# Kernel optimization log

Hardware: AMD Instinct MI355X
Metric: run time of the kernel (lower is better)

Reference implementation:

```python
import jax, jax.numpy as jnp
import numpy as np

N, D_IN, D_OUT, E = 8192, 2048, 8192, 8


def setup_inputs() -> dict:
    key = jax.random.key(0)
    k1, k2, k3 = jax.random.split(key, 3)
    x = jax.random.normal(k1, (N, D_IN), dtype=jnp.float32)
    # packed weight layout [E, in, out] (pack() pretransposes [E,out,in] -> [E,in,out])
    weight = jax.random.normal(k2, (E, D_IN, D_OUT), dtype=jnp.float32) * (1.0 / np.sqrt(D_IN))
    indices = jax.random.randint(k3, (N,), 0, E, dtype=jnp.int32)
    return {"x": x, "weight": weight, "indices": indices}


def reference(x, weight, indices):
    # gather_mm: out[n] = x[n] @ weight[indices[n]]  -> [N, D_OUT]
    # Avoid materializing weight[indices] ([N, in, out]); instead loop over the
    # small fixed expert count, masking tokens routed to each expert.
    n_experts = weight.shape[0]
    out = jnp.zeros((x.shape[0], weight.shape[-1]), dtype=x.dtype)
    for e in range(n_experts):
        mask = (indices == e)[:, None]
        xe = jnp.where(mask, x, 0)          # zero out tokens not routed to e
        out = out + xe @ weight[e]           # [N, in] @ [in, out]
    return out
```

## Files before the change

kernel.cpp:

```cpp
#include <hip/hip_runtime.h>
#include <hip/hip_bf16.h>
#include <stdint.h>

#define N_TOK 8192
#define D_IN  2048
#define D_OUT 8192
#define NEXP  8
#define KST   32
#define NT2   40
#define NS2   32
#define AIMG  32768
#define X_OFF2 65536
#define X_BYTES2 ((long)NT2 * KST * AIMG)
#define W_OFF2 (X_OFF2 + X_BYTES2)
#define W_BYTES2 ((long)NEXP * NS2 * KST * AIMG)
#define WS_NEED2 ((size_t)(W_OFF2 + W_BYTES2))
#define NWIMG (NEXP * 64 * KST)


typedef float  f32x4  __attribute__((ext_vector_type(4)));
typedef __bf16 bf16x8 __attribute__((ext_vector_type(8)));

__global__ void SwitchLinear_setup_kernel(const int* __restrict__ idx,
                                          int* __restrict__ ws) {
    __shared__ int cnt[NEXP], cur[NEXP];
    int t = threadIdx.x;
    if (t < NEXP) cnt[t] = 0;
    __syncthreads();
    for (int i = t; i < N_TOK; i += 256) atomicAdd(&cnt[idx[i]], 1);
    __syncthreads();
    if (t == 0) {
        int o = 0, nt = 0, nt1 = 0;
        for (int e = 0; e < NEXP; ++e) {
            cur[e] = o;
            int c = cnt[e];
            for (int r = 0; r < c; r += 256) {
                ws[8 + nt]   = e;
                ws[96 + nt]  = o + r;
                ws[192 + nt] = (c - r < 256) ? (c - r) : 256;
                ++nt;
            }
            for (int r = 0; r < c; r += 128) {
                ws[256 + nt1] = e;
                ws[328 + nt1] = o + r;
                ws[400 + nt1] = (c - r < 128) ? (c - r) : 128;
                ++nt1;
            }
            o += c;
        }
        ws[0] = nt;
        ws[4] = nt1;
    }
    __syncthreads();
    for (int i = t; i < N_TOK; i += 256) {
        int p = atomicAdd(&cur[idx[i]], 1);
        ws[512 + p] = i;
    }
}

__global__ __launch_bounds__(256) void SwitchLinear_conv_kernel(
    const float* __restrict__ x, const float* __restrict__ w,
    const int* __restrict__ ws, char* __restrict__ wsb) {
    const int bidx = blockIdx.x;
    const int t = threadIdx.x;
    if (bidx < NWIMG) {
        const int img = bidx;
        const int kst = img & 31, s = (img >> 5) & 63, e = img >> 11;
        const int y = s >> 1, hh = s & 1;
        __shared__ float tl[64 * 129];
        const float* src = w + (long)e * D_IN * D_OUT + (long)(kst * 64) * D_OUT +
                           y * 256 + hh * 128;
#pragma unroll
        for (int i = 0; i < 8; ++i) {
            int u = t + i * 256;
            int row = u >> 5, ch = u & 31;
            f32x4 v = *(const f32x4*)(src + (long)row * D_OUT + ch * 4);
            float* d = &tl[row * 129 + ch * 4];
            d[0] = v[0]; d[1] = v[1]; d[2] = v[2]; d[3] = v[3];
        }
        __syncthreads();
        char* dimg = wsb + W_OFF2 + (long)((e * NS2 + y) * KST + kst) * AIMG;
#pragma unroll
        for (int i = 0; i < 4; ++i) {
            int u = t + i * 256;
            int cl = u >> 3, kc8 = u & 7;
            union { __bf16 h8[8]; uint4 u4; } c;
#pragma unroll
            for (int j = 0; j < 8; ++j) c.h8[j] = (__bf16)tl[(kc8 * 8 + j) * 129 + cl];
            int cc = hh * 128 + cl;
            int slot = (((cc & 1) << 2) | (kc8 & 3)) ^ ((cc >> 1) & 7);
            *(uint4*)(dimg + (kc8 >> 2) * 16384 + ((cc >> 1) << 7) + (slot << 4)) = c.u4;
        }
    } else {
        const int u2 = bidx - NWIMG;
        const int tile = u2 % NT2, kst = u2 / NT2;
        if (tile >= ws[0]) return;
        const int rs = ws[96 + tile], rows = ws[192 + tile];
        char* img = wsb + X_OFF2 + (long)(tile * KST + kst) * AIMG;
#pragma unroll
        for (int i = 0; i < 8; ++i) {
            int u = t + i * 256;
            int R = u >> 3, kc8 = u & 7;
            int rl = rs + (R < rows ? R : rows - 1);
            int token = ws[512 + rl];
            const float* src = x + (long)token * D_IN + kst * 64 + kc8 * 8;
            f32x4 v0 = *(const f32x4*)src;
            f32x4 v1 = *(const f32x4*)(src + 4);
            union { __bf16 hh[8]; uint4 u4; } c;
            c.hh[0] = (__bf16)v0[0]; c.hh[1] = (__bf16)v0[1];
            c.hh[2] = (__bf16)v0[2]; c.hh[3] = (__bf16)v0[3];
            c.hh[4] = (__bf16)v1[0]; c.hh[5] = (__bf16)v1[1];
            c.hh[6] = (__bf16)v1[2]; c.hh[7] = (__bf16)v1[3];
            int slot = (((R & 1) << 2) | (kc8 & 3)) ^ ((R >> 1) & 7);
            *(uint4*)(img + (kc8 >> 2) * 16384 + ((R >> 1) << 7) + (slot << 4)) = c.u4;
        }
    }
}


__global__ __launch_bounds__(512, 1) void SwitchLinear_gemm_kernel(
    const char* __restrict__ wsb, const int* __restrict__ ws,
    float* __restrict__ out) {
    const int bid = blockIdx.x;
    const int lb  = (bid & 7) * ((NT2 * NS2) / 8) + (bid >> 3);
    const int tx  = lb % NT2;
    const int y   = lb / NT2;
    if (tx >= ws[0]) return;
    const int e = ws[8 + tx], rs = ws[96 + tx], rows = ws[192 + tx];

    __shared__ __align__(16) char lds[2][2][2][16384];
    __shared__ int ord[256];

    const int t = threadIdx.x;
    if (t < 256) ord[t] = ws[512 + rs + (t < rows ? t : 0)];
    __syncthreads();

    const char* aImg = wsb + X_OFF2 + (long)(tx * KST) * AIMG;
    const char* bImg = wsb + W_OFF2 + (long)((e * NS2 + y) * KST) * AIMG;

    const int lane = t & 63;
    const int wid  = t >> 6;
    const int wr = wid >> 2, wc = wid & 3;
    const int lm = lane & 15, lk = lane >> 4;

    f32x4 acc[8][4];
#pragma unroll
    for (int i = 0; i < 8; ++i)
#pragma unroll
        for (int j = 0; j < 4; ++j) acc[i][j] = (f32x4){0.f, 0.f, 0.f, 0.f};

    bf16x8 aa[4], bb[4];

#define STG(op, ks, half, tt)                                                 \
    __builtin_amdgcn_global_load_lds(                                         \
        (const __attribute__((address_space(1))) uint32_t*)(                  \
            ((op) ? bImg : aImg) + (long)(tt) * AIMG + (ks) * 16384 +         \
            (half) * 8192 + t * 16),                                          \
        (__attribute__((address_space(3))) uint32_t*)(                        \
            &lds[(tt) & 1][op][ks][(half) * 8192 + t * 16]),                  \
        16, 0, 0)

#define SWB(r) ((((r) >> 1) << 7) + (((((((r) & 1) << 2)) | lk) ^ (((r) >> 1) & 7)) << 4))

#define LDB(p, ks)                                                            \
    do { _Pragma("unroll")                                                    \
        for (int ni = 0; ni < 4; ++ni) {                                      \
            int cc = wc * 64 + ni * 16 + lm;                                  \
            bb[ni] = *(const bf16x8*)(&lds[p][1][ks][SWB(cc)]);               \
        } } while (0)

#define LDA(p, ks, mh)                                                        \
    do { _Pragma("unroll")                                                    \
        for (int q = 0; q < 4; ++q) {                                         \
            int rr = wr * 128 + (mh) * 64 + q * 16 + lm;                      \
            aa[q] = *(const bf16x8*)(&lds[p][0][ks][SWB(rr)]);                \
        } } while (0)

#define MFMA16(mh)                                                            \
    do { _Pragma("unroll")                                                    \
        for (int q = 0; q < 4; ++q)                                           \
            _Pragma("unroll")                                                 \
            for (int ni = 0; ni < 4; ++ni)                                    \
                acc[(mh) * 4 + q][ni] = __builtin_amdgcn_mfma_f32_16x16x32_bf16( \
                    aa[q], bb[ni], acc[(mh) * 4 + q][ni], 0, 0, 0);           \
    } while (0)

#define PH(p, ks, mh, DOB, ISSUE, POST)                                       \
    do {                                                                      \
        if (DOB) LDB(p, ks);                                                  \
        LDA(p, ks, mh);                                                       \
        ISSUE;                                                                \
        __builtin_amdgcn_s_barrier();                                         \
        asm volatile("s_waitcnt lgkmcnt(0)" ::: "memory");                    \
        __builtin_amdgcn_sched_barrier(0);                                    \
        __builtin_amdgcn_s_setprio(1);                                        \
        MFMA16(mh);                                                           \
        __builtin_amdgcn_s_setprio(0);                                        \
        POST;                                                                 \
        __builtin_amdgcn_s_barrier();                                         \
    } while (0)

    STG(0, 0, 0, 0); STG(0, 0, 1, 0); STG(1, 0, 0, 0); STG(1, 0, 1, 0);
    STG(0, 1, 0, 0); STG(0, 1, 1, 0); STG(1, 1, 0, 0); STG(1, 1, 1, 0);
    asm volatile("s_waitcnt vmcnt(4)" ::: "memory");
    __builtin_amdgcn_s_barrier();

    for (int tt = 0; tt < KST - 1; ++tt) {
        const int p = tt & 1;
        const int nx = tt + 1;
        PH(p, 0, 0, 1, { STG(0, 0, 0, nx); STG(0, 0, 1, nx); }, ((void)0));
        PH(p, 0, 1, 0, { STG(1, 0, 0, nx); STG(1, 0, 1, nx); },
           asm volatile("s_waitcnt vmcnt(4)" ::: "memory"));
        PH(p, 1, 0, 1, { STG(0, 1, 0, nx); STG(0, 1, 1, nx); }, ((void)0));
        PH(p, 1, 1, 0, { STG(1, 1, 0, nx); STG(1, 1, 1, nx); },
           asm volatile("s_waitcnt vmcnt(4)" ::: "memory"));
    }
    {
        const int p = (KST - 1) & 1;
        PH(p, 0, 0, 1, ((void)0), ((void)0));
        PH(p, 0, 1, 0, ((void)0),
           asm volatile("s_waitcnt vmcnt(0)" ::: "memory"));
        PH(p, 1, 0, 1, ((void)0), ((void)0));
        PH(p, 1, 1, 0, ((void)0), ((void)0));
    }

#pragma unroll
    for (int mi = 0; mi < 8; ++mi) {
#pragma unroll
        for (int j = 0; j < 4; ++j) {
            int rl = wr * 128 + mi * 16 + lk * 4 + j;
            if (rl < rows) {
                int token = ord[rl];
                float* po = out + (long)token * D_OUT + y * 256 + wc * 64 + lm;
#pragma unroll
                for (int ni = 0; ni < 4; ++ni) po[ni * 16] = acc[mi][ni][j];
            }
        }
    }
#undef STG
#undef SWB
#undef LDB
#undef LDA
#undef MFMA16
#undef PH
}


__device__ __forceinline__ int fb_a_byte(int r, int kbyte) {
    return r * 128 + (kbyte ^ ((r & 7) << 4));
}
__device__ __forceinline__ int fb_b_byte(int n, int kbyte) {
    int slot = (n ^ (n >> 2)) & 7;
    return n * 128 + (kbyte ^ (slot << 4));
}

__global__ __launch_bounds__(256, 2) void SwitchLinear_gemm_fb_kernel(
    const float* __restrict__ x, const float* __restrict__ w,
    const int* __restrict__ ws, float* __restrict__ out) {
    const int nt = ws[4];
    const int tx = blockIdx.x;
    if (tx >= nt) return;
    const int e    = ws[256 + tx];
    const int rs   = ws[328 + tx];
    const int rows = ws[400 + tx];
    const int col0 = blockIdx.y * 128;

    __shared__ __align__(16) unsigned short As[128 * 64];
    __shared__ __align__(16) unsigned short Bs[128 * 64];
    __shared__ int ord[128];

    const int t = threadIdx.x;
    if (t < 128) {
        int r = (t < rows) ? (rs + t) : rs;
        ord[t] = ws[512 + r];
    }
    __syncthreads();

    const int kq = t & 15;
    const float* pA[8];
    int rowA[8];
#pragma unroll
    for (int i = 0; i < 8; ++i) {
        int r = (t >> 4) + 16 * i;
        rowA[i] = r;
        pA[i] = x + (long)ord[r] * D_IN + kq * 4;
    }
    const float* pB[2];
    int nB[2], kbB[2];
#pragma unroll
    for (int i = 0; i < 2; ++i) {
        int u = t + 256 * i;
        int kgf = u >> 5, q = u & 31;
        kbB[i] = kgf * 4;
        nB[i]  = q * 4;
        pB[i]  = w + (long)e * D_IN * D_OUT + (long)(kgf * 4) * D_OUT + col0 + q * 4;
    }

    const int lane = t & 63;
    const int wid  = t >> 6;
    const int wr = wid >> 1, wc = wid & 1;
    const int lm = lane & 15, lk = lane >> 4;

    f32x4 acc[4][4];
#pragma unroll
    for (int i = 0; i < 4; ++i)
#pragma unroll
        for (int j = 0; j < 4; ++j) acc[i][j] = (f32x4){0.f, 0.f, 0.f, 0.f};

    for (int k0 = 0; k0 < D_IN; k0 += 64) {
#pragma unroll
        for (int i = 0; i < 8; ++i) {
            f32x4 v = *(const f32x4*)(pA[i] + k0);
            union { __bf16 h[4]; uint2 u; } c;
            c.h[0] = (__bf16)v[0]; c.h[1] = (__bf16)v[1];
            c.h[2] = (__bf16)v[2]; c.h[3] = (__bf16)v[3];
            *(uint2*)((char*)As + fb_a_byte(rowA[i], kq * 8)) = c.u;
        }
#pragma unroll
        for (int i = 0; i < 2; ++i) {
            const float* p = pB[i] + (long)k0 * D_OUT;
            f32x4 r0 = *(const f32x4*)(p);
            f32x4 r1 = *(const f32x4*)(p + D_OUT);
            f32x4 r2 = *(const f32x4*)(p + 2 * D_OUT);
            f32x4 r3 = *(const f32x4*)(p + 3 * D_OUT);
#pragma unroll
            for (int j = 0; j < 4; ++j) {
                int n = nB[i] + j;
                union { __bf16 h[4]; uint2 u; } c;
                c.h[0] = (__bf16)r0[j]; c.h[1] = (__bf16)r1[j];
                c.h[2] = (__bf16)r2[j]; c.h[3] = (__bf16)r3[j];
                *(uint2*)((char*)Bs + fb_b_byte(n, kbB[i] * 2)) = c.u;
            }
        }
        __syncthreads();
#pragma unroll
        for (int ks = 0; ks < 2; ++ks) {
            bf16x8 a[4], b[4];
            const int kbyte = ks * 64 + lk * 16;
#pragma unroll
            for (int mi = 0; mi < 4; ++mi) {
                int r = wr * 64 + mi * 16 + lm;
                a[mi] = *(const bf16x8*)((const char*)As + fb_a_byte(r, kbyte));
            }
#pragma unroll
            for (int ni = 0; ni < 4; ++ni) {
                int n = wc * 64 + ni * 16 + lm;
                b[ni] = *(const bf16x8*)((const char*)Bs + fb_b_byte(n, kbyte));
            }
#pragma unroll
            for (int mi = 0; mi < 4; ++mi)
#pragma unroll
                for (int ni = 0; ni < 4; ++ni)
                    acc[mi][ni] = __builtin_amdgcn_mfma_f32_16x16x32_bf16(
                        a[mi], b[ni], acc[mi][ni], 0, 0, 0);
        }
        __syncthreads();
    }
#pragma unroll
    for (int mi = 0; mi < 4; ++mi) {
#pragma unroll
        for (int j = 0; j < 4; ++j) {
            int rl = wr * 64 + mi * 16 + lk * 4 + j;
            if (rl < rows) {
                int token = ord[rl];
                float* po = out + (long)token * D_OUT + col0 + wc * 64 + lm;
#pragma unroll
                for (int ni = 0; ni < 4; ++ni) po[ni * 16] = acc[mi][ni][j];
            }
        }
    }
}

extern "C" void kernel_launch(void* const* d_in, const int* in_sizes, int n_in,
                              void* d_out, int out_size, void* d_ws, size_t ws_size,
                              hipStream_t stream) {
    const float* x   = (const float*)d_in[0];
    const float* w   = (const float*)d_in[1];
    const int*   idx = (const int*)d_in[2];
    float* out = (float*)d_out;
    int*   ws  = (int*)d_ws;
    char*  wsb = (char*)d_ws;

    SwitchLinear_setup_kernel<<<1, 256, 0, stream>>>(idx, ws);
    if (ws_size >= WS_NEED2) {
        SwitchLinear_conv_kernel<<<NWIMG + NT2 * KST, 256, 0, stream>>>(x, w, ws, wsb);
        SwitchLinear_gemm_kernel<<<NT2 * NS2, 512, 0, stream>>>(wsb, ws, out);
    } else {
        dim3 grid(72, 64);
        SwitchLinear_gemm_fb_kernel<<<grid, 256, 0, stream>>>(x, w, ws, out);
    }
}
```

Baseline: 553.0 us.

## Shrink GEMM tile to 128x128 with 256 threads and two blocks per CU

The main GEMM moves from 256x256 tiles with 512 threads and one block per CU to 128x128 tiles with 256 threads and two blocks per CU. Each tile reads its half of the existing bf16 X and W images, using a new per-tile image index computed in setup. The token order list moves to offset 1024 so the new index table has room. This is meant to reduce padding waste on partial expert tiles and improve load balance and occupancy, at the cost of lower data reuse per tile and more global traffic.

```diff
diff --git a/kernel.cpp b/kernel.cpp
--- a/kernel.cpp
+++ b/kernel.cpp
@@ -8,7 +8,9 @@
 #define NEXP  8
 #define KST   32
 #define NT2   40
+#define NT1G  72
 #define NS2   32
+#define NS1   64
 #define AIMG  32768
 #define X_OFF2 65536
 #define X_BYTES2 ((long)NT2 * KST * AIMG)
@@ -16,6 +18,7 @@
 #define W_BYTES2 ((long)NEXP * NS2 * KST * AIMG)
 #define WS_NEED2 ((size_t)(W_OFF2 + W_BYTES2))
 #define NWIMG (NEXP * 64 * KST)
+#define GRID1 (NT1G * NS1)
 
 
 typedef float  f32x4  __attribute__((ext_vector_type(4)));
@@ -34,17 +37,20 @@
         for (int e = 0; e < NEXP; ++e) {
             cur[e] = o;
             int c = cnt[e];
+            const int T0 = nt;
             for (int r = 0; r < c; r += 256) {
                 ws[8 + nt]   = e;
                 ws[96 + nt]  = o + r;
                 ws[192 + nt] = (c - r < 256) ? (c - r) : 256;
                 ++nt;
             }
+            int j = 0;
             for (int r = 0; r < c; r += 128) {
                 ws[256 + nt1] = e;
                 ws[328 + nt1] = o + r;
                 ws[400 + nt1] = (c - r < 128) ? (c - r) : 128;
-                ++nt1;
+                ws[472 + nt1] = (T0 + (j >> 1)) * 2 + (j & 1);
+                ++nt1; ++j;
             }
             o += c;
         }
@@ -54,7 +60,7 @@
     __syncthreads();
     for (int i = t; i < N_TOK; i += 256) {
         int p = atomicAdd(&cur[idx[i]], 1);
-        ws[512 + p] = i;
+        ws[1024 + p] = i;
     }
 }
 
@@ -102,7 +108,7 @@
             int u = t + i * 256;
             int R = u >> 3, kc8 = u & 7;
             int rl = rs + (R < rows ? R : rows - 1);
-            int token = ws[512 + rl];
+            int token = ws[1024 + rl];
             const float* src = x + (long)token * D_IN + kst * 64 + kc8 * 8;
             f32x4 v0 = *(const f32x4*)src;
             f32x4 v1 = *(const f32x4*)(src + 4);
@@ -118,127 +124,133 @@
 }
 
 
-__global__ __launch_bounds__(512, 1) void SwitchLinear_gemm_kernel(
+__global__ __launch_bounds__(256, 2) void SwitchLinear_gemm_kernel(
     const char* __restrict__ wsb, const int* __restrict__ ws,
     float* __restrict__ out) {
     const int bid = blockIdx.x;
-    const int lb  = (bid & 7) * ((NT2 * NS2) / 8) + (bid >> 3);
-    const int tx  = lb % NT2;
-    const int y   = lb / NT2;
-    if (tx >= ws[0]) return;
-    const int e = ws[8 + tx], rs = ws[96 + tx], rows = ws[192 + tx];
-
-    __shared__ __align__(16) char lds[2][2][2][16384];
-    __shared__ int ord[256];
+    const int lb  = (bid & 7) * (GRID1 / 8) + (bid >> 3);
+    const int tx  = lb % NT1G;
+    const int y   = lb / NT1G;
+    if (tx >= ws[4]) return;
+    const int e = ws[256 + tx], rs = ws[328 + tx], rows = ws[400 + tx];
+    const int img = ws[472 + tx];
+
+    __shared__ __align__(16) char ldsA[2][2][8192];
+    __shared__ __align__(16) char ldsB[2][2][8192];
+    __shared__ int ord[128];
 
     const int t = threadIdx.x;
-    if (t < 256) ord[t] = ws[512 + rs + (t < rows ? t : 0)];
+    if (t < 128) ord[t] = ws[1024 + rs + (t < rows ? t : 0)];
     __syncthreads();
 
-    const char* aImg = wsb + X_OFF2 + (long)(tx * KST) * AIMG;
-    const char* bImg = wsb + W_OFF2 + (long)((e * NS2 + y) * KST) * AIMG;
+    const char* aBase = wsb + X_OFF2 + (long)((img >> 1) * KST) * AIMG + (img & 1) * 8192;
+    const char* bBase = wsb + W_OFF2 + (long)((e * NS2 + (y >> 1)) * KST) * AIMG +
+                        (y & 1) * 8192;
 
     const int lane = t & 63;
     const int wid  = t >> 6;
-    const int wr = wid >> 2, wc = wid & 3;
+    const int wr = wid >> 1, wc = wid & 1;
     const int lm = lane & 15, lk = lane >> 4;
 
-    f32x4 acc[8][4];
-#pragma unroll
-    for (int i = 0; i < 8; ++i)
+    f32x4 acc[4][4];
+#pragma unroll
+    for (int i = 0; i < 4; ++i)
 #pragma unroll
         for (int j = 0; j < 4; ++j) acc[i][j] = (f32x4){0.f, 0.f, 0.f, 0.f};
 
     bf16x8 aa[4], bb[4];
 
-#define STG(op, ks, half, tt)                                                 \
+#define STGA(ks, o2, tt)                                                      \
     __builtin_amdgcn_global_load_lds(                                         \
         (const __attribute__((address_space(1))) uint32_t*)(                  \
-            ((op) ? bImg : aImg) + (long)(tt) * AIMG + (ks) * 16384 +         \
-            (half) * 8192 + t * 16),                                          \
+            aBase + (long)(tt) * AIMG + (ks) * 16384 + (o2) * 4096 + t * 16), \
         (__attribute__((address_space(3))) uint32_t*)(                        \
-            &lds[(tt) & 1][op][ks][(half) * 8192 + t * 16]),                  \
+            &ldsA[(tt) & 1][ks][(o2) * 4096 + t * 16]),                       \
         16, 0, 0)
 
-#define SWB(r) ((((r) >> 1) << 7) + (((((((r) & 1) << 2)) | lk) ^ (((r) >> 1) & 7)) << 4))
+#define STGB(ks, o2, tt)                                                      \
+    __builtin_amdgcn_global_load_lds(                                         \
+        (const __attribute__((address_space(1))) uint32_t*)(                  \
+            bBase + (long)(tt) * AIMG + (ks) * 16384 + (o2) * 4096 + t * 16), \
+        (__attribute__((address_space(3))) uint32_t*)(                        \
+            &ldsB[(tt) & 1][ks][(o2) * 4096 + t * 16]),                       \
+        16, 0, 0)
+
+#define SWBH(r) ((((r) >> 1) << 7) + (((((((r) & 1) << 2)) | lk) ^ (((r) >> 1) & 7)) << 4))
 
 #define LDB(p, ks)                                                            \
     do { _Pragma("unroll")                                                    \
         for (int ni = 0; ni < 4; ++ni) {                                      \
             int cc = wc * 64 + ni * 16 + lm;                                  \
-            bb[ni] = *(const bf16x8*)(&lds[p][1][ks][SWB(cc)]);               \
+            bb[ni] = *(const bf16x8*)(&ldsB[p][ks][SWBH(cc)]);                \
         } } while (0)
 
-#define LDA(p, ks, mh)                                                        \
+#define LDA(p, ks)                                                            \
     do { _Pragma("unroll")                                                    \
         for (int q = 0; q < 4; ++q) {                                         \
-            int rr = wr * 128 + (mh) * 64 + q * 16 + lm;                      \
-            aa[q] = *(const bf16x8*)(&lds[p][0][ks][SWB(rr)]);                \
+            int rr = wr * 64 + q * 16 + lm;                                   \
+            aa[q] = *(const bf16x8*)(&ldsA[p][ks][SWBH(rr)]);                 \
         } } while (0)
 
-#define MFMA16(mh)                                                            \
+#define MFMA16()                                                              \
     do { _Pragma("unroll")                                                    \
         for (int q = 0; q < 4; ++q)                                           \
             _Pragma("unroll")                                                 \
             for (int ni = 0; ni < 4; ++ni)                                    \
-                acc[(mh) * 4 + q][ni] = __builtin_amdgcn_mfma_f32_16x16x32_bf16( \
-                    aa[q], bb[ni], acc[(mh) * 4 + q][ni], 0, 0, 0);           \
+                acc[q][ni] = __builtin_amdgcn_mfma_f32_16x16x32_bf16(         \
+                    aa[q], bb[ni], acc[q][ni], 0, 0, 0);                      \
     } while (0)
 
-#define PH(p, ks, mh, DOB, ISSUE, POST)                                       \
+#define PH(p, ks, ISSUE, POST)                                                \
     do {                                                                      \
-        if (DOB) LDB(p, ks);                                                  \
-        LDA(p, ks, mh);                                                       \
+        LDB(p, ks);                                                           \
+        LDA(p, ks);                                                           \
         ISSUE;                                                                \
         __builtin_amdgcn_s_barrier();                                         \
         asm volatile("s_waitcnt lgkmcnt(0)" ::: "memory");                    \
         __builtin_amdgcn_sched_barrier(0);                                    \
         __builtin_amdgcn_s_setprio(1);                                        \
-        MFMA16(mh);                                                           \
+        MFMA16();                                                             \
         __builtin_amdgcn_s_setprio(0);                                        \
         POST;                                                                 \
         __builtin_amdgcn_s_barrier();                                         \
     } while (0)
 
-    STG(0, 0, 0, 0); STG(0, 0, 1, 0); STG(1, 0, 0, 0); STG(1, 0, 1, 0);
-    STG(0, 1, 0, 0); STG(0, 1, 1, 0); STG(1, 1, 0, 0); STG(1, 1, 1, 0);
+    STGA(0, 0, 0); STGA(0, 1, 0); STGB(0, 0, 0); STGB(0, 1, 0);
+    STGA(1, 0, 0); STGA(1, 1, 0); STGB(1, 0, 0); STGB(1, 1, 0);
     asm volatile("s_waitcnt vmcnt(4)" ::: "memory");
     __builtin_amdgcn_s_barrier();
 
     for (int tt = 0; tt < KST - 1; ++tt) {
         const int p = tt & 1;
         const int nx = tt + 1;
-        PH(p, 0, 0, 1, { STG(0, 0, 0, nx); STG(0, 0, 1, nx); }, ((void)0));
-        PH(p, 0, 1, 0, { STG(1, 0, 0, nx); STG(1, 0, 1, nx); },
+        PH(p, 0, { STGA(0, 0, nx); STGA(0, 1, nx); STGB(0, 0, nx); STGB(0, 1, nx); },
            asm volatile("s_waitcnt vmcnt(4)" ::: "memory"));
-        PH(p, 1, 0, 1, { STG(0, 1, 0, nx); STG(0, 1, 1, nx); }, ((void)0));
-        PH(p, 1, 1, 0, { STG(1, 1, 0, nx); STG(1, 1, 1, nx); },
+        PH(p, 1, { STGA(1, 0, nx); STGA(1, 1, nx); STGB(1, 0, nx); STGB(1, 1, nx); },
            asm volatile("s_waitcnt vmcnt(4)" ::: "memory"));
     }
     {
         const int p = (KST - 1) & 1;
-        PH(p, 0, 0, 1, ((void)0), ((void)0));
-        PH(p, 0, 1, 0, ((void)0),
-           asm volatile("s_waitcnt vmcnt(0)" ::: "memory"));
-        PH(p, 1, 0, 1, ((void)0), ((void)0));
-        PH(p, 1, 1, 0, ((void)0), ((void)0));
-    }
-
-#pragma unroll
-    for (int mi = 0; mi < 8; ++mi) {
+        PH(p, 0, ((void)0), asm volatile("s_waitcnt vmcnt(0)" ::: "memory"));
+        PH(p, 1, ((void)0), ((void)0));
+    }
+
+#pragma unroll
+    for (int mi = 0; mi < 4; ++mi) {
 #pragma unroll
         for (int j = 0; j < 4; ++j) {
-            int rl = wr * 128 + mi * 16 + lk * 4 + j;
+            int rl = wr * 64 + mi * 16 + lk * 4 + j;
             if (rl < rows) {
                 int token = ord[rl];
-                float* po = out + (long)token * D_OUT + y * 256 + wc * 64 + lm;
+                float* po = out + (long)token * D_OUT + y * 128 + wc * 64 + lm;
 #pragma unroll
                 for (int ni = 0; ni < 4; ++ni) po[ni * 16] = acc[mi][ni][j];
             }
         }
     }
-#undef STG
-#undef SWB
+#undef STGA
+#undef STGB
+#undef SWBH
 #undef LDB
 #undef LDA
 #undef MFMA16
@@ -272,7 +284,7 @@
     const int t = threadIdx.x;
     if (t < 128) {
         int r = (t < rows) ? (rs + t) : rs;
-        ord[t] = ws[512 + r];
+        ord[t] = ws[1024 + r];
     }
     __syncthreads();
 
@@ -384,9 +396,9 @@
     SwitchLinear_setup_kernel<<<1, 256, 0, stream>>>(idx, ws);
     if (ws_size >= WS_NEED2) {
         SwitchLinear_conv_kernel<<<NWIMG + NT2 * KST, 256, 0, stream>>>(x, w, ws, wsb);
-        SwitchLinear_gemm_kernel<<<NT2 * NS2, 512, 0, stream>>>(wsb, ws, out);
+        SwitchLinear_gemm_kernel<<<GRID1, 256, 0, stream>>>(wsb, ws, out);
     } else {
-        dim3 grid(72, 64);
+        dim3 grid(NT1G, NS1);
         SwitchLinear_gemm_fb_kernel<<<grid, 256, 0, stream>>>(x, w, ws, out);
     }
 }
```

New measurement: 654.2 us. 1.18x slower.
